# Kernel tuning notes

Measured on AMD Instinct MI355X. Metric: run time of the kernel, lower is better.

Reference implementation:

```python
import jax, jax.numpy as jnp
import numpy as np

B, N, S, P, D = 128, 4096, 32, 64, 128  # batch, wafers, stages, PMs, embed dim
NORM = 300.0


def gather(src, idx):
    # src: [B, n, D], idx: [B, m] int -> [B, m, D]
    return jnp.take_along_axis(src, idx[:, :, None], axis=1)


def setup_inputs() -> dict:
    key = jax.random.key(0)
    ks = jax.random.split(key, 16)
    return {
        "encoded_row": jax.random.normal(ks[0], (B, N, D), jnp.float32),
        "encoded_col": jax.random.normal(ks[1], (B, S, D), jnp.float32),
        "clock": jax.random.uniform(ks[2], (B, 1), jnp.float32) * NORM,
        "loc_process_end_time": jax.random.uniform(ks[3], (B, P), jnp.float32) * (2.0 * NORM),
        "W_dyn": jax.random.normal(ks[4], (2, D), jnp.float32) * 0.05,
        "W_concat": jax.random.normal(ks[5], (3 * D, D), jnp.float32) * 0.05,
        "W_robot": jax.random.normal(ks[6], (3 * D, D), jnp.float32) * 0.05,
        "loc_hold_wafer": jax.random.randint(ks[7], (B, P), 0, N),
        "loc_stage": jax.random.randint(ks[8], (B, P), 1, S + 1),
        "robot_arm1_loc": jax.random.randint(ks[9], (B, 1), 0, P + 2),
        "robot_arm2_loc": jax.random.randint(ks[10], (B, 1), 0, P + 2),
        "arm1_recipe": jax.random.randint(ks[11], (B, 1), 0, N),
        "arm2_recipe": jax.random.randint(ks[12], (B, 1), 0, N),
        "arm1_next_stage": jax.random.randint(ks[13], (B, 1), 0, S + 2),
        "arm2_next_stage": jax.random.randint(ks[14], (B, 1), 0, S + 2),
    }


def reference(encoded_row, encoded_col, clock, loc_process_end_time,
              W_dyn, W_concat, W_robot,
              loc_hold_wafer, loc_stage, robot_arm1_loc, robot_arm2_loc,
              arm1_recipe, arm2_recipe, arm1_next_stage, arm2_next_stage):
    dt = encoded_row.dtype
    # ---- get_PM_embedding ----
    clk = jnp.broadcast_to(clock, (B, P))
    remain_prs = jnp.where(loc_process_end_time > clk,
                           loc_process_end_time - clk, 0.0) / NORM
    remain_purge = jnp.zeros_like(remain_prs)
    pm_dyn = jnp.stack([remain_prs, remain_purge], axis=-1) @ W_dyn  # [B,P,D]

    rows_dummy = jnp.concatenate(
        [encoded_row, jnp.zeros((B, 1, D), dt)], axis=1)          # [B,N+1,D]
    lot_idx = jnp.where(loc_hold_wafer >= 0, loc_hold_wafer, N)
    pm_wafer = gather(rows_dummy, lot_idx)                         # [B,P,D]
    pm_stage = gather(encoded_col, loc_stage - 1)                  # [B,P,D]
    pm_emb = jnp.concatenate([pm_stage, pm_wafer, pm_dyn], -1) @ W_concat

    # ---- get_robot_embedding ----
    loc_emb = jnp.concatenate(
        [jnp.zeros((B, 1, D), dt), pm_emb, jnp.ones((B, 1, D), dt)], axis=1)
    cols_pad = jnp.concatenate(
        [jnp.zeros((B, 1, D), dt), encoded_col, jnp.zeros((B, 1, D), dt)], axis=1)

    def arm_embed(loc_idx, recipe, next_stage):
        a_loc = gather(loc_emb, loc_idx)                           # [B,1,D]
        a_wafer = gather(rows_dummy, jnp.where(recipe >= 0, recipe, N))
        a_ns = gather(cols_pad, jnp.where(next_stage >= 0, next_stage, 0))
        return jnp.concatenate([a_loc, a_wafer, a_ns], -1) @ W_robot

    arm1 = arm_embed(robot_arm1_loc, arm1_recipe, arm1_next_stage)
    arm2 = arm_embed(robot_arm2_loc, arm2_recipe, arm2_next_stage)

    return jnp.concatenate([pm_emb, arm1, arm2], axis=1)           # [B,P+2,D]
```

## Files before the change

### kernel.cpp

```cpp
#include <hip/hip_runtime.h>
#include <stdint.h>

namespace {
constexpr int B = 128;
constexpr int N = 4096;
constexpr int S = 32;
constexpr int P = 64;
constexpr int D = 128;
constexpr int K = 384;
constexpr int ROWS = 8;
}

__device__ __forceinline__ uint32_t f2bf(float f) {
    union { float f; uint32_t u; } v; v.f = f;
    return (v.u + 0x7FFFu + ((v.u >> 16) & 1u)) >> 16;
}
__device__ __forceinline__ uint32_t pack2(float x, float y) {
    return f2bf(x) | (f2bf(y) << 16);
}
__device__ __forceinline__ float blo(uint32_t u) {
    union { uint32_t u; float f; } t; t.u = u << 16; return t.f;
}
__device__ __forceinline__ float bhi(uint32_t u) {
    union { uint32_t u; float f; } t; t.u = u & 0xFFFF0000u; return t.f;
}

__global__ __launch_bounds__(64) void pm_emb_kernel(
    const float* __restrict__ enc_row,
    const float* __restrict__ enc_col,
    const float* __restrict__ clockp,
    const float* __restrict__ lpet,
    const float* __restrict__ W_dyn,
    const float* __restrict__ W_concat,
    const int*   __restrict__ lhw,
    const int*   __restrict__ lstage,
    float* __restrict__ out)
{
    __shared__ uint32_t xs[ROWS][K / 2];
    const int lane = threadIdx.x;
    const int r0 = blockIdx.x * ROWS;

    #pragma unroll
    for (int r = 0; r < ROWS; ++r) {
        const int rid = r0 + r;
        const int b = rid >> 6;
        const float c = clockp[b];
        const float t = lpet[rid];
        const float rem = (t > c) ? (t - c) * (1.0f / 300.0f) : 0.0f;
        const int wi = lhw[rid];
        const int cs = lstage[rid] - 1;

        float2 sv = ((const float2*)(enc_col + ((size_t)b * S + cs) * D))[lane];
        float2 wv = make_float2(0.f, 0.f);
        if (wi >= 0)
            wv = ((const float2*)(enc_row + ((size_t)b * N + wi) * D))[lane];
        float2 dv = ((const float2*)W_dyn)[lane];

        xs[r][0 * 64 + lane] = pack2(sv.x, sv.y);
        xs[r][1 * 64 + lane] = pack2(wv.x, wv.y);
        xs[r][2 * 64 + lane] = pack2(dv.x * rem, dv.y * rem);
    }
    __syncthreads();

    float acc0[ROWS], acc1[ROWS];
    #pragma unroll
    for (int r = 0; r < ROWS; ++r) { acc0[r] = 0.f; acc1[r] = 0.f; }

    for (int kc = 0; kc < K / 8; ++kc) {
        float w0[8], w1[8];
        #pragma unroll
        for (int kk = 0; kk < 8; ++kk) {
            w0[kk] = W_concat[(kc * 8 + kk) * D + lane];
            w1[kk] = W_concat[(kc * 8 + kk) * D + lane + 64];
        }
        #pragma unroll
        for (int r = 0; r < ROWS; ++r) {
            const uint4 xq = *(const uint4*)&xs[r][kc * 4];
            float xv[8];
            xv[0] = blo(xq.x); xv[1] = bhi(xq.x);
            xv[2] = blo(xq.y); xv[3] = bhi(xq.y);
            xv[4] = blo(xq.z); xv[5] = bhi(xq.z);
            xv[6] = blo(xq.w); xv[7] = bhi(xq.w);
            #pragma unroll
            for (int kk = 0; kk < 8; ++kk) {
                acc0[r] = fmaf(xv[kk], w0[kk], acc0[r]);
                acc1[r] = fmaf(xv[kk], w1[kk], acc1[r]);
            }
        }
    }

    #pragma unroll
    for (int r = 0; r < ROWS; ++r) {
        const int rid = r0 + r;
        const int b = rid >> 6;
        const int p = rid & 63;
        const size_t o = ((size_t)b * (P + 2) + p) * D + lane;
        out[o] = acc0[r];
        out[o + 64] = acc1[r];
    }
}

__global__ __launch_bounds__(64) void arm_kernel(
    const float* __restrict__ enc_row,
    const float* __restrict__ enc_col,
    const float* __restrict__ W_robot,
    const int* __restrict__ loc1, const int* __restrict__ loc2,
    const int* __restrict__ rec1, const int* __restrict__ rec2,
    const int* __restrict__ nst1, const int* __restrict__ nst2,
    float* __restrict__ out)
{
    __shared__ uint32_t xs[K / 2];
    const int lane = threadIdx.x;
    const int b = blockIdx.x >> 1;
    const int arm = blockIdx.x & 1;
    const int loc = arm ? loc2[b] : loc1[b];
    const int rec = arm ? rec2[b] : rec1[b];
    int ns = arm ? nst2[b] : nst1[b];
    if (ns < 0) ns = 0;

    float2 lv = make_float2(0.f, 0.f);
    if (loc >= 1 && loc <= P)
        lv = ((const float2*)(out + ((size_t)b * (P + 2) + (loc - 1)) * D))[lane];
    else if (loc == P + 1)
        lv = make_float2(1.f, 1.f);
    float2 wv = make_float2(0.f, 0.f);
    if (rec >= 0)
        wv = ((const float2*)(enc_row + ((size_t)b * N + rec) * D))[lane];
    float2 nv = make_float2(0.f, 0.f);
    if (ns >= 1 && ns <= S)
        nv = ((const float2*)(enc_col + ((size_t)b * S + (ns - 1)) * D))[lane];

    xs[0 * 64 + lane] = pack2(lv.x, lv.y);
    xs[1 * 64 + lane] = pack2(wv.x, wv.y);
    xs[2 * 64 + lane] = pack2(nv.x, nv.y);
    __syncthreads();

    float acc0 = 0.f, acc1 = 0.f;
    for (int kc = 0; kc < K / 8; ++kc) {
        const uint4 xq = *(const uint4*)&xs[kc * 4];
        float xv[8];
        xv[0] = blo(xq.x); xv[1] = bhi(xq.x);
        xv[2] = blo(xq.y); xv[3] = bhi(xq.y);
        xv[4] = blo(xq.z); xv[5] = bhi(xq.z);
        xv[6] = blo(xq.w); xv[7] = bhi(xq.w);
        #pragma unroll
        for (int kk = 0; kk < 8; ++kk) {
            const float w0 = W_robot[(kc * 8 + kk) * D + lane];
            const float w1 = W_robot[(kc * 8 + kk) * D + lane + 64];
            acc0 = fmaf(xv[kk], w0, acc0);
            acc1 = fmaf(xv[kk], w1, acc1);
        }
    }
    const size_t o = ((size_t)b * (P + 2) + P + arm) * D + lane;
    out[o] = acc0;
    out[o + 64] = acc1;
}

extern "C" void kernel_launch(void* const* d_in, const int* in_sizes, int n_in,
                              void* d_out, int out_size, void* d_ws, size_t ws_size,
                              hipStream_t stream) {
    const float* enc_row  = (const float*)d_in[0];
    const float* enc_col  = (const float*)d_in[1];
    const float* clockp   = (const float*)d_in[2];
    const float* lpet     = (const float*)d_in[3];
    const float* W_dyn    = (const float*)d_in[4];
    const float* W_concat = (const float*)d_in[5];
    const float* W_robot  = (const float*)d_in[6];
    const int*   lhw      = (const int*)d_in[7];
    const int*   lstage   = (const int*)d_in[8];
    const int*   loc1     = (const int*)d_in[9];
    const int*   loc2     = (const int*)d_in[10];
    const int*   rec1     = (const int*)d_in[11];
    const int*   rec2     = (const int*)d_in[12];
    const int*   nst1     = (const int*)d_in[13];
    const int*   nst2     = (const int*)d_in[14];
    float* out = (float*)d_out;

    pm_emb_kernel<<<(B * P) / ROWS, 64, 0, stream>>>(
        enc_row, enc_col, clockp, lpet, W_dyn, W_concat, lhw, lstage, out);
    arm_kernel<<<2 * B, 64, 0, stream>>>(
        enc_row, enc_col, W_robot, loc1, loc2, rec1, rec2, nst1, nst2, out);
}
```

Measured before the change: 383.0 us.

## Use bf16 MFMA for PM embedding GEMM with pre-swizzled weights

Replaces the scalar-FMA per-lane dot product in the PM embedding kernel with 16x16x32 bf16 MFMA instructions. A new prep kernel packs W_concat into bf16 in an MFMA-friendly swizzled layout in workspace. Each 256-thread block now computes 16 rows with four waves, each wave covering 32 output columns. This adds an extra launch and a workspace write per call, and it changes the shared-memory padding and the output store pattern.

```diff
diff --git a/kernel.cpp b/kernel.cpp
--- a/kernel.cpp
+++ b/kernel.cpp
@@ -8,8 +8,12 @@
 constexpr int P = 64;
 constexpr int D = 128;
 constexpr int K = 384;
-constexpr int ROWS = 8;
-}
+constexpr int KS = K / 32;
+constexpr int ROWPAD = 196;
+}
+
+typedef __attribute__((ext_vector_type(8))) short short8;
+typedef __attribute__((ext_vector_type(4))) float f32x4;
 
 __device__ __forceinline__ uint32_t f2bf(float f) {
     union { float f; uint32_t u; } v; v.f = f;
@@ -25,78 +29,91 @@
     union { uint32_t u; float f; } t; t.u = u & 0xFFFF0000u; return t.f;
 }
 
-__global__ __launch_bounds__(64) void pm_emb_kernel(
+__global__ __launch_bounds__(256) void prep_w_kernel(
+    const float* __restrict__ W, uint32_t* __restrict__ Wsw)
+{
+    const int idx = blockIdx.x * 256 + threadIdx.x;
+    const int n  = idx & 15;
+    const int t  = (idx >> 4) & 7;
+    const int q  = (idx >> 7) & 3;
+    const int ks = idx >> 9;
+    const int col  = t * 16 + n;
+    const int krow = ks * 32 + q * 8;
+    uint32_t pk[4];
+    #pragma unroll
+    for (int jj = 0; jj < 4; ++jj) {
+        const float a = W[(size_t)(krow + 2 * jj) * D + col];
+        const float b = W[(size_t)(krow + 2 * jj + 1) * D + col];
+        pk[jj] = pack2(a, b);
+    }
+    ((uint4*)Wsw)[idx] = make_uint4(pk[0], pk[1], pk[2], pk[3]);
+}
+
+__global__ __launch_bounds__(256) void pm_gemm_kernel(
     const float* __restrict__ enc_row,
     const float* __restrict__ enc_col,
     const float* __restrict__ clockp,
     const float* __restrict__ lpet,
     const float* __restrict__ W_dyn,
-    const float* __restrict__ W_concat,
     const int*   __restrict__ lhw,
     const int*   __restrict__ lstage,
+    const uint32_t* __restrict__ Wsw,
     float* __restrict__ out)
 {
-    __shared__ uint32_t xs[ROWS][K / 2];
-    const int lane = threadIdx.x;
-    const int r0 = blockIdx.x * ROWS;
-
-    #pragma unroll
-    for (int r = 0; r < ROWS; ++r) {
+    __shared__ uint32_t xs[16 * ROWPAD];
+    const int lane = threadIdx.x & 63;
+    const int wave = threadIdx.x >> 6;
+    const int r0 = blockIdx.x * 16;
+
+    const float2 wd = ((const float2*)W_dyn)[lane];
+    #pragma unroll
+    for (int rr = 0; rr < 4; ++rr) {
+        const int r = wave * 4 + rr;
         const int rid = r0 + r;
         const int b = rid >> 6;
         const float c = clockp[b];
-        const float t = lpet[rid];
-        const float rem = (t > c) ? (t - c) * (1.0f / 300.0f) : 0.0f;
+        const float tt = lpet[rid];
+        const float rem = (tt > c) ? (tt - c) * (1.0f / 300.0f) : 0.0f;
         const int wi = lhw[rid];
         const int cs = lstage[rid] - 1;
 
-        float2 sv = ((const float2*)(enc_col + ((size_t)b * S + cs) * D))[lane];
+        const float2 sv = ((const float2*)(enc_col + ((size_t)b * S + cs) * D))[lane];
         float2 wv = make_float2(0.f, 0.f);
         if (wi >= 0)
             wv = ((const float2*)(enc_row + ((size_t)b * N + wi) * D))[lane];
-        float2 dv = ((const float2*)W_dyn)[lane];
-
-        xs[r][0 * 64 + lane] = pack2(sv.x, sv.y);
-        xs[r][1 * 64 + lane] = pack2(wv.x, wv.y);
-        xs[r][2 * 64 + lane] = pack2(dv.x * rem, dv.y * rem);
+
+        xs[r * ROWPAD + 0 * 64 + lane] = pack2(sv.x, sv.y);
+        xs[r * ROWPAD + 1 * 64 + lane] = pack2(wv.x, wv.y);
+        xs[r * ROWPAD + 2 * 64 + lane] = pack2(wd.x * rem, wd.y * rem);
     }
     __syncthreads();
 
-    float acc0[ROWS], acc1[ROWS];
-    #pragma unroll
-    for (int r = 0; r < ROWS; ++r) { acc0[r] = 0.f; acc1[r] = 0.f; }
-
-    for (int kc = 0; kc < K / 8; ++kc) {
-        float w0[8], w1[8];
-        #pragma unroll
-        for (int kk = 0; kk < 8; ++kk) {
-            w0[kk] = W_concat[(kc * 8 + kk) * D + lane];
-            w1[kk] = W_concat[(kc * 8 + kk) * D + lane + 64];
-        }
-        #pragma unroll
-        for (int r = 0; r < ROWS; ++r) {
-            const uint4 xq = *(const uint4*)&xs[r][kc * 4];
-            float xv[8];
-            xv[0] = blo(xq.x); xv[1] = bhi(xq.x);
-            xv[2] = blo(xq.y); xv[3] = bhi(xq.y);
-            xv[4] = blo(xq.z); xv[5] = bhi(xq.z);
-            xv[6] = blo(xq.w); xv[7] = bhi(xq.w);
-            #pragma unroll
-            for (int kk = 0; kk < 8; ++kk) {
-                acc0[r] = fmaf(xv[kk], w0[kk], acc0[r]);
-                acc1[r] = fmaf(xv[kk], w1[kk], acc1[r]);
-            }
-        }
-    }
-
-    #pragma unroll
-    for (int r = 0; r < ROWS; ++r) {
-        const int rid = r0 + r;
-        const int b = rid >> 6;
-        const int p = rid & 63;
-        const size_t o = ((size_t)b * (P + 2) + p) * D + lane;
-        out[o] = acc0[r];
-        out[o + 64] = acc1[r];
+    const int q = lane >> 4;
+    const int n16 = lane & 15;
+    const int t0 = wave * 2, t1 = t0 + 1;
+
+    f32x4 acc0 = {0.f, 0.f, 0.f, 0.f};
+    f32x4 acc1 = {0.f, 0.f, 0.f, 0.f};
+    const short8* wsw = (const short8*)Wsw;
+
+    #pragma unroll
+    for (int ks = 0; ks < KS; ++ks) {
+        const short8 a = *(const short8*)(xs + n16 * ROWPAD + ks * 16 + q * 4);
+        const short8 b0 = wsw[((ks * 4 + q) * 8 + t0) * 16 + n16];
+        const short8 b1 = wsw[((ks * 4 + q) * 8 + t1) * 16 + n16];
+        acc0 = __builtin_amdgcn_mfma_f32_16x16x32_bf16(a, b0, acc0, 0, 0, 0);
+        acc1 = __builtin_amdgcn_mfma_f32_16x16x32_bf16(a, b1, acc1, 0, 0, 0);
+    }
+
+    #pragma unroll
+    for (int i = 0; i < 4; ++i) {
+        const int row = q * 4 + i;
+        const int rid = r0 + row;
+        const int bb = rid >> 6;
+        const int pp = rid & 63;
+        float* o = out + ((size_t)bb * (P + 2) + pp) * D;
+        o[t0 * 16 + n16] = acc0[i];
+        o[t1 * 16 + n16] = acc1[i];
     }
 }
 
@@ -175,9 +192,11 @@
     const int*   nst1     = (const int*)d_in[13];
     const int*   nst2     = (const int*)d_in[14];
     float* out = (float*)d_out;
-
-    pm_emb_kernel<<<(B * P) / ROWS, 64, 0, stream>>>(
-        enc_row, enc_col, clockp, lpet, W_dyn, W_concat, lhw, lstage, out);
+    uint32_t* Wsw = (uint32_t*)d_ws;
+
+    prep_w_kernel<<<24, 256, 0, stream>>>(W_concat, Wsw);
+    pm_gemm_kernel<<<(B * P) / 16, 256, 0, stream>>>(
+        enc_row, enc_col, clockp, lpet, W_dyn, lhw, lstage, Wsw, out);
     arm_kernel<<<2 * B, 64, 0, stream>>>(
         enc_row, enc_col, W_robot, loc1, loc2, rec1, rec2, nst1, nst2, out);
 }
```

Result: faster. 340.5 us (-11.1%).
